# Performance work log

Measured on AMD Instinct MI355X. Metric: run time of the kernel, lower is better.

## Reference

```python
import jax, jax.numpy as jnp
import numpy as np

N_MEMBERS = 2      # ensemble_length=3, loop runs i=1..2
N_NODES = 65536    # batch_size * total_length = 32 * 2048
N_EDGES = 1_048_576
N_LAYERS = 12      # num_conv_layers
D = 64             # constant feature width (linspace 64->64)


def setup_inputs() -> dict:
    key = jax.random.key(0)
    k0, k1, k2, k3 = jax.random.split(key, 4)
    x = jax.random.normal(k0, (N_MEMBERS, N_NODES, D), dtype=jnp.float32)
    edge_index = jax.random.randint(k1, (N_MEMBERS, 2, N_EDGES), 0, N_NODES, dtype=jnp.int64)
    # GCNConv weights per member/layer; scale ~ 1/sqrt(D) for stability across 12 layers
    W = jax.random.normal(k2, (N_MEMBERS, N_LAYERS, D, D), dtype=jnp.float32) / jnp.sqrt(jnp.float32(D))
    b = jax.random.normal(k3, (N_MEMBERS, N_LAYERS, D), dtype=jnp.float32) * 0.01
    return {"x": x, "edge_index": edge_index, "W": W, "b": b}


def gcn_conv(h, src, dst, W, b):
    """PyG GCNConv: add self-loops, symmetric D^-1/2 (A+I) D^-1/2 normalization,
    linear transform, bias."""
    hw = h @ W                                                # [N, D_out]
    # degree includes the self-loop (+1)
    deg = jax.ops.segment_sum(jnp.ones((src.shape[0],), h.dtype), dst,
                              num_segments=N_NODES) + jnp.asarray(1.0, h.dtype)
    dinv = jax.lax.rsqrt(deg)                                 # [N]
    norm = dinv[src] * dinv[dst]                              # [E]
    agg = jax.ops.segment_sum(norm[:, None] * hw[src], dst, num_segments=N_NODES)
    agg = agg + (dinv * dinv)[:, None] * hw                   # self-loop term
    return agg + b


def reference(x, edge_index, W, b):
    # eval mode: F.dropout(training=False) is identity
    outs = []
    for i in range(N_MEMBERS):
        src, dst = edge_index[i, 0], edge_index[i, 1]
        h = x[i]
        for j in range(N_LAYERS - 1):
            h = jax.nn.relu(gcn_conv(h, src, dst, W[i, j], b[i, j]))
        outs.append(gcn_conv(h, src, dst, W[i, N_LAYERS - 1], b[i, N_LAYERS - 1]))
    return jnp.stack(outs)  # [N_MEMBERS, N_NODES, D]
```

## Files before the change

kernel.cpp:

```cpp
#include <hip/hip_runtime.h>
#include <hip/hip_fp16.h>
#include <math.h>

#define N_MEMBERS 2
#define N_NODES   65536
#define N_EDGES   1048576
#define N_LAYERS  12
#define D         64
#define OFF_STRIDE (N_NODES + 1)
#define NODE_MASK (N_NODES - 1)

#define NBINS       256
#define BIN_CAP     5120
#define EDGES_PER_WG 4096

typedef _Float16 f16;
typedef f16   f16x8 __attribute__((ext_vector_type(8)));
typedef float f32x4 __attribute__((ext_vector_type(4)));


__global__ __launch_bounds__(256) void bin_scatter_k(const int* __restrict__ ei,
                                                     int* __restrict__ binCursor,
                                                     unsigned int* __restrict__ binned) {
    int m = blockIdx.y;
    int t = threadIdx.x;
    int eBase = blockIdx.x * EDGES_PER_WG;
    __shared__ int hist[NBINS];
    __shared__ int base[NBINS];
    hist[t] = 0;
    __syncthreads();
    const int* srcp = ei + (size_t)(m * 2 + 0) * N_EDGES;
    const int* dstp = ei + (size_t)(m * 2 + 1) * N_EDGES;
    unsigned int pk[16];
    int bn[16], rk[16];
    #pragma unroll
    for (int i = 0; i < 16; i++) {
        int e = eBase + i * 256 + t;
        int src = srcp[e] & NODE_MASK;
        int dst = dstp[e] & NODE_MASK;
        int b = dst >> 8;
        bn[i] = b;
        pk[i] = ((unsigned)src << 8) | (unsigned)(dst & 255);
        rk[i] = atomicAdd(&hist[b], 1);
    }
    __syncthreads();
    base[t] = atomicAdd(&binCursor[m * NBINS + t], hist[t]);
    __syncthreads();
    unsigned int* bb = binned + (size_t)m * NBINS * BIN_CAP;
    #pragma unroll
    for (int i = 0; i < 16; i++) {
        int pos = base[bn[i]] + rk[i];
        if (pos < BIN_CAP)
            bb[(size_t)bn[i] * BIN_CAP + pos] = pk[i];
    }
}

__global__ __launch_bounds__(256) void scan_bins_k(const int* __restrict__ cur,
                                                   int* __restrict__ bbase) {
    int m = blockIdx.x, t = threadIdx.x;
    __shared__ int sh[256];
    int v0 = cur[m * NBINS + t];
    sh[t] = v0;
    __syncthreads();
    for (int ofs = 1; ofs < 256; ofs <<= 1) {
        int v = sh[t];
        int a = (t >= ofs) ? sh[t - ofs] : 0;
        __syncthreads();
        sh[t] = v + a;
        __syncthreads();
    }
    bbase[m * NBINS + t] = sh[t] - v0;
}

__global__ __launch_bounds__(256) void bin_build_k(const unsigned int* __restrict__ binned,
                                                   const int* __restrict__ binCursor,
                                                   const int* __restrict__ bbase,
                                                   int* __restrict__ off,
                                                   float* __restrict__ dinv,
                                                   unsigned short* __restrict__ csr_src) {
    int m = blockIdx.y, b = blockIdx.x, t = threadIdx.x;
    int cnt   = binCursor[m * NBINS + b];
    int gbase = bbase[m * NBINS + b];
    const unsigned int* bb = binned + ((size_t)m * NBINS + b) * BIN_CAP;
    __shared__ int degl[256];
    __shared__ int offl[256];
    degl[t] = 0;
    __syncthreads();
    unsigned int ed[20];
    #pragma unroll
    for (int j = 0; j < 20; j++) {
        int i = t + j * 256;
        ed[j] = 0;
        if (i < cnt) {
            unsigned int w = bb[i];
            int r = atomicAdd(&degl[w & 255], 1);
            ed[j] = w | ((unsigned)r << 24);
        }
    }
    __syncthreads();
    int myDeg = degl[t];
    offl[t] = myDeg;
    __syncthreads();
    for (int ofs = 1; ofs < 256; ofs <<= 1) {
        int v = offl[t];
        int a = (t >= ofs) ? offl[t - ofs] : 0;
        __syncthreads();
        offl[t] = v + a;
        __syncthreads();
    }
    int myOff = gbase + offl[t] - myDeg;
    int node = b * 256 + t;
    off[m * OFF_STRIDE + node] = myOff;
    if (b == NBINS - 1 && t == 255) off[m * OFF_STRIDE + N_NODES] = N_EDGES;
    dinv[m * N_NODES + node] = 1.0f / sqrtf((float)myDeg + 1.0f);
    offl[t] = myOff;
    __syncthreads();
    unsigned short* cs = csr_src + (size_t)m * N_EDGES;
    #pragma unroll
    for (int j = 0; j < 20; j++) {
        int i = t + j * 256;
        if (i < cnt) {
            int dl  = ed[j] & 255;
            int src = (ed[j] >> 8) & 0xFFFF;
            int r   = ed[j] >> 24;
            cs[offl[dl] + r] = (unsigned short)src;
        }
    }
}

__global__ __launch_bounds__(256) void prescale_k(const float* __restrict__ x,
                                                  const float* __restrict__ dinv,
                                                  __half* __restrict__ g) {
    int i = blockIdx.x * 256 + threadIdx.x;
    float dv = dinv[i >> 3];
    float4 a = ((const float4*)x)[i * 2];
    float4 b = ((const float4*)x)[i * 2 + 1];
    union { __half2 h2[4]; uint4 u; } p;
    p.h2[0] = __floats2half2_rn(dv * a.x, dv * a.y);
    p.h2[1] = __floats2half2_rn(dv * a.z, dv * a.w);
    p.h2[2] = __floats2half2_rn(dv * b.x, dv * b.y);
    p.h2[3] = __floats2half2_rn(dv * b.z, dv * b.w);
    ((uint4*)g)[i] = p.u;
}

__device__ __forceinline__ void cvt8(uint4 u, float* f) {
    const __half2* h2 = (const __half2*)&u;
    #pragma unroll
    for (int i = 0; i < 4; i++) {
        float2 t = __half22float2(h2[i]);
        f[2 * i]     = t.x;
        f[2 * i + 1] = t.y;
    }
}

__global__ __launch_bounds__(256) void aggregate_k(const __half* __restrict__ g,
                                                   __half* __restrict__ S,
                                                   const int* __restrict__ off,
                                                   const unsigned short* __restrict__ csr_src,
                                                   const float* __restrict__ dinv) {
    int bflat = blockIdx.x;
    int xcd   = bflat & 7;
    int m     = xcd >> 2;
    int slot  = ((bflat >> 3) << 2) | (xcd & 3);
    int wav   = threadIdx.x >> 6;
    int nA    = slot * 8 + wav * 2;
    int nB    = nA + 1;
    int lane = threadIdx.x & 63;
    int fg   = lane & 7;
    int sub  = lane >> 3;
    const __half*         gm = g + (size_t)m * N_NODES * D;
    const int*            ob = off + m * OFF_STRIDE;
    const unsigned short* sb = csr_src + (size_t)m * N_EDGES;

    float accA[8], accB[8];
    #pragma unroll
    for (int i = 0; i < 8; i++) { accA[i] = 0.f; accB[i] = 0.f; }

    int eA0 = ob[nA], eA1 = ob[nA + 1], eB1 = ob[nB + 1];
    int eB0 = eA1;
    #pragma unroll 2
    for (int eA = eA0, eB = eB0; (eA < eA1) || (eB < eB1); eA += 8, eB += 8) {
        int ia = eA + sub, ib = eB + sub;
        int idxA = (ia < eA1) ? ia : (eA1 - 1);
        int idxB = (ib < eB1) ? ib : (eB1 - 1);
        float wA = (ia < eA1) ? 1.0f : 0.0f;
        float wB = (ib < eB1) ? 1.0f : 0.0f;
        int sA = sb[idxA];
        int sB = sb[idxB];
        uint4 gA = *(const uint4*)(gm + (size_t)sA * D + fg * 8);
        uint4 gB = *(const uint4*)(gm + (size_t)sB * D + fg * 8);
        float fA[8], fB[8];
        cvt8(gA, fA);
        cvt8(gB, fB);
        #pragma unroll
        for (int i = 0; i < 8; i++) {
            accA[i] = fmaf(wA, fA[i], accA[i]);
            accB[i] = fmaf(wB, fB[i], accB[i]);
        }
    }
    #pragma unroll
    for (int msk = 8; msk < 64; msk <<= 1)
        #pragma unroll
        for (int i = 0; i < 8; i++) {
            accA[i] += __shfl_xor(accA[i], msk);
            accB[i] += __shfl_xor(accB[i], msk);
        }

    float dvA = dinv[m * N_NODES + nA];
    float dvB = dinv[m * N_NODES + nB];
    uint4 sgA = *(const uint4*)(gm + (size_t)nA * D + fg * 8);
    uint4 sgB = *(const uint4*)(gm + (size_t)nB * D + fg * 8);
    float sfA[8], sfB[8];
    cvt8(sgA, sfA);
    cvt8(sgB, sfB);
    __half* Sm = S + (size_t)m * N_NODES * D;
    if (sub == 0) {
        union { __half2 h2[4]; uint4 u; } p;
        #pragma unroll
        for (int i = 0; i < 4; i++)
            p.h2[i] = __floats2half2_rn(dvA * (accA[2 * i]     + sfA[2 * i]),
                                        dvA * (accA[2 * i + 1] + sfA[2 * i + 1]));
        *(uint4*)(Sm + (size_t)nA * D + fg * 8) = p.u;
    } else if (sub == 1) {
        union { __half2 h2[4]; uint4 u; } p;
        #pragma unroll
        for (int i = 0; i < 4; i++)
            p.h2[i] = __floats2half2_rn(dvB * (accB[2 * i]     + sfB[2 * i]),
                                        dvB * (accB[2 * i + 1] + sfB[2 * i + 1]));
        *(uint4*)(Sm + (size_t)nB * D + fg * 8) = p.u;
    }
}

__global__ __launch_bounds__(256) void gemm_f16_k(const __half* __restrict__ S,
                                                  const float* __restrict__ Wall,
                                                  const float* __restrict__ dinv,
                                                  const float* __restrict__ ball,
                                                  __half* __restrict__ gout,
                                                  float* __restrict__ fout,
                                                  int layer, int last) {
    int m = blockIdx.y;
    const float* Wg = Wall + (size_t)(m * N_LAYERS + layer) * D * D;
    __shared__ __align__(16) _Float16 Whi[D][72];
    __shared__ __align__(16) _Float16 Wlo[D][72];
    for (int idx = threadIdx.x; idx < D * D / 4; idx += 256) {
        float4 v = ((const float4*)Wg)[idx];
        int k  = idx >> 4;
        int c0 = (idx & 15) << 2;
        float vv[4] = {v.x, v.y, v.z, v.w};
        #pragma unroll
        for (int i = 0; i < 4; i++) {
            f16 hi = (f16)vv[i];
            Whi[c0 + i][k] = hi;
            Wlo[c0 + i][k] = (f16)(vv[i] - (float)hi);
        }
    }
    __syncthreads();

    int lane = threadIdx.x & 63;
    int wav  = threadIdx.x >> 6;
    int nn   = lane & 15;
    int quad = lane >> 4;

    f16x8 Bh[8], Bl[8];
    #pragma unroll
    for (int t = 0; t < 4; t++)
        #pragma unroll
        for (int s = 0; s < 2; s++) {
            Bh[t * 2 + s] = *(const f16x8*)&Whi[t * 16 + nn][s * 32 + quad * 8];
            Bl[t * 2 + s] = *(const f16x8*)&Wlo[t * 16 + nn][s * 32 + quad * 8];
        }

    const __half* Sm = S + (size_t)m * N_NODES * D;
    const float*  dm = dinv + m * N_NODES;
    const float*  bp = ball + (size_t)(m * N_LAYERS + layer) * D;
    __half*       gm = gout + (size_t)m * N_NODES * D;
    float*        fm = fout + (size_t)m * N_NODES * D;

    float4 b4[4];
    #pragma unroll
    for (int t = 0; t < 4; t++)
        b4[t] = *(const float4*)(bp + t * 16 + quad * 4);

    int base = blockIdx.x * 128 + wav * 32;
    #pragma unroll
    for (int g = 0; g < 2; g++) {
        int node = base + g * 16 + nn;
        const __half* srow = Sm + (size_t)node * D;
        f16x8 a0 = *(const f16x8*)(srow + quad * 8);
        f16x8 a1 = *(const f16x8*)(srow + 32 + quad * 8);
        float dv = dm[node];
        #pragma unroll
        for (int t = 0; t < 4; t++) {
            f32x4 c = {0.f, 0.f, 0.f, 0.f};
            c = __builtin_amdgcn_mfma_f32_16x16x32_f16(Bh[t * 2 + 0], a0, c, 0, 0, 0);
            c = __builtin_amdgcn_mfma_f32_16x16x32_f16(Bh[t * 2 + 1], a1, c, 0, 0, 0);
            c = __builtin_amdgcn_mfma_f32_16x16x32_f16(Bl[t * 2 + 0], a0, c, 0, 0, 0);
            c = __builtin_amdgcn_mfma_f32_16x16x32_f16(Bl[t * 2 + 1], a1, c, 0, 0, 0);
            float v0 = (float)c[0] + b4[t].x;
            float v1 = (float)c[1] + b4[t].y;
            float v2 = (float)c[2] + b4[t].z;
            float v3 = (float)c[3] + b4[t].w;
            int col = t * 16 + quad * 4;
            if (last) {
                *(float4*)(fm + (size_t)node * D + col) = make_float4(v0, v1, v2, v3);
            } else {
                union { __half2 h2[2]; uint2 u; } p;
                p.h2[0] = __floats2half2_rn(fmaxf(v0, 0.f) * dv, fmaxf(v1, 0.f) * dv);
                p.h2[1] = __floats2half2_rn(fmaxf(v2, 0.f) * dv, fmaxf(v3, 0.f) * dv);
                *(uint2*)(gm + (size_t)node * D + col) = p.u;
            }
        }
    }
}


extern "C" void kernel_launch(void* const* d_in, const int* in_sizes, int n_in,
                              void* d_out, int out_size, void* d_ws, size_t ws_size,
                              hipStream_t stream) {
    (void)in_sizes; (void)n_in; (void)out_size; (void)ws_size;
    const float* x  = (const float*)d_in[0];
    const int*   ei = (const int*)d_in[1];
    const float* W  = (const float*)d_in[2];
    const float* b  = (const float*)d_in[3];
    float* out = (float*)d_out;

    char* ws = (char*)d_ws;
    size_t o = 0;
    auto take = [&](size_t bytes) -> void* {
        void* p = ws + o;
        o = (o + bytes + 255) & ~(size_t)255;
        return p;
    };
    float*          dinv      = (float*) take((size_t)N_MEMBERS * N_NODES * 4);
    int*            off       = (int*)   take((size_t)N_MEMBERS * OFF_STRIDE * 4);
    int*            binCursor = (int*)   take((size_t)N_MEMBERS * NBINS * 4);
    int*            bbase     = (int*)   take((size_t)N_MEMBERS * NBINS * 4);
    unsigned short* csr_src   = (unsigned short*)take((size_t)N_MEMBERS * N_EDGES * 2);
    __half*         gbuf      = (__half*)take((size_t)N_MEMBERS * N_NODES * D * 2);
    __half*         Sbuf      = (__half*)take((size_t)N_MEMBERS * N_NODES * D * 2);
    unsigned int*   binned    = (unsigned int*)Sbuf;

    hipMemsetAsync(binCursor, 0, (size_t)N_MEMBERS * NBINS * 4, stream);

    bin_scatter_k<<<dim3(N_EDGES / EDGES_PER_WG, N_MEMBERS), 256, 0, stream>>>(
        ei, binCursor, binned);
    scan_bins_k<<<dim3(N_MEMBERS), 256, 0, stream>>>(binCursor, bbase);
    bin_build_k<<<dim3(NBINS, N_MEMBERS), 256, 0, stream>>>(
        binned, binCursor, bbase, off, dinv, csr_src);
    prescale_k<<<dim3((N_MEMBERS * N_NODES * D / 8) / 256), 256, 0, stream>>>(
        x, dinv, gbuf);

    for (int j = 0; j < N_LAYERS; j++) {
        aggregate_k<<<dim3(N_MEMBERS * (N_NODES / 8)), 256, 0, stream>>>(
            gbuf, Sbuf, off, csr_src, dinv);
        gemm_f16_k<<<dim3(N_NODES / 128, N_MEMBERS), 256, 0, stream>>>(
            Sbuf, W, dinv, b, gbuf, out, j, (j == N_LAYERS - 1) ? 1 : 0);
    }
}
```

Before: 806.5 us.

## Fuse aggregation and GEMM into one per-layer kernel via shared-memory tile

Merges the sparse aggregation kernel and the dense f16 MFMA GEMM into a single layer kernel. Each block aggregates 32 nodes into a shared-memory tile, then multiplies it by the split hi/lo weights and writes the activated, prescaled output to a ping-pong buffer. This removes the global write and re-read of the intermediate S buffer and halves kernel launches per layer. In exchange, every block reloads and converts the 64x64 weight matrix (2048 blocks instead of 1024), and each wave processes 8 nodes serially, which lowers latency hiding in the gather phase.

```diff
diff --git a/kernel.cpp b/kernel.cpp
--- a/kernel.cpp
+++ b/kernel.cpp
@@ -153,95 +153,26 @@
     }
 }
 
-__global__ __launch_bounds__(256) void aggregate_k(const __half* __restrict__ g,
-                                                   __half* __restrict__ S,
-                                                   const int* __restrict__ off,
-                                                   const unsigned short* __restrict__ csr_src,
-                                                   const float* __restrict__ dinv) {
+__global__ __launch_bounds__(256) void layer_k(const __half* __restrict__ g,
+                                               const float* __restrict__ Wall,
+                                               const float* __restrict__ dinv,
+                                               const float* __restrict__ ball,
+                                               const int* __restrict__ off,
+                                               const unsigned short* __restrict__ csr_src,
+                                               __half* __restrict__ gout,
+                                               float* __restrict__ fout,
+                                               int layer, int last) {
+    __shared__ __align__(16) _Float16 Whi[D][72];
+    __shared__ __align__(16) _Float16 Wlo[D][72];
+    __shared__ __align__(16) _Float16 Sl[32][72];
+
     int bflat = blockIdx.x;
     int xcd   = bflat & 7;
     int m     = xcd >> 2;
     int slot  = ((bflat >> 3) << 2) | (xcd & 3);
-    int wav   = threadIdx.x >> 6;
-    int nA    = slot * 8 + wav * 2;
-    int nB    = nA + 1;
-    int lane = threadIdx.x & 63;
-    int fg   = lane & 7;
-    int sub  = lane >> 3;
-    const __half*         gm = g + (size_t)m * N_NODES * D;
-    const int*            ob = off + m * OFF_STRIDE;
-    const unsigned short* sb = csr_src + (size_t)m * N_EDGES;
-
-    float accA[8], accB[8];
-    #pragma unroll
-    for (int i = 0; i < 8; i++) { accA[i] = 0.f; accB[i] = 0.f; }
-
-    int eA0 = ob[nA], eA1 = ob[nA + 1], eB1 = ob[nB + 1];
-    int eB0 = eA1;
-    #pragma unroll 2
-    for (int eA = eA0, eB = eB0; (eA < eA1) || (eB < eB1); eA += 8, eB += 8) {
-        int ia = eA + sub, ib = eB + sub;
-        int idxA = (ia < eA1) ? ia : (eA1 - 1);
-        int idxB = (ib < eB1) ? ib : (eB1 - 1);
-        float wA = (ia < eA1) ? 1.0f : 0.0f;
-        float wB = (ib < eB1) ? 1.0f : 0.0f;
-        int sA = sb[idxA];
-        int sB = sb[idxB];
-        uint4 gA = *(const uint4*)(gm + (size_t)sA * D + fg * 8);
-        uint4 gB = *(const uint4*)(gm + (size_t)sB * D + fg * 8);
-        float fA[8], fB[8];
-        cvt8(gA, fA);
-        cvt8(gB, fB);
-        #pragma unroll
-        for (int i = 0; i < 8; i++) {
-            accA[i] = fmaf(wA, fA[i], accA[i]);
-            accB[i] = fmaf(wB, fB[i], accB[i]);
-        }
-    }
-    #pragma unroll
-    for (int msk = 8; msk < 64; msk <<= 1)
-        #pragma unroll
-        for (int i = 0; i < 8; i++) {
-            accA[i] += __shfl_xor(accA[i], msk);
-            accB[i] += __shfl_xor(accB[i], msk);
-        }
-
-    float dvA = dinv[m * N_NODES + nA];
-    float dvB = dinv[m * N_NODES + nB];
-    uint4 sgA = *(const uint4*)(gm + (size_t)nA * D + fg * 8);
-    uint4 sgB = *(const uint4*)(gm + (size_t)nB * D + fg * 8);
-    float sfA[8], sfB[8];
-    cvt8(sgA, sfA);
-    cvt8(sgB, sfB);
-    __half* Sm = S + (size_t)m * N_NODES * D;
-    if (sub == 0) {
-        union { __half2 h2[4]; uint4 u; } p;
-        #pragma unroll
-        for (int i = 0; i < 4; i++)
-            p.h2[i] = __floats2half2_rn(dvA * (accA[2 * i]     + sfA[2 * i]),
-                                        dvA * (accA[2 * i + 1] + sfA[2 * i + 1]));
-        *(uint4*)(Sm + (size_t)nA * D + fg * 8) = p.u;
-    } else if (sub == 1) {
-        union { __half2 h2[4]; uint4 u; } p;
-        #pragma unroll
-        for (int i = 0; i < 4; i++)
-            p.h2[i] = __floats2half2_rn(dvB * (accB[2 * i]     + sfB[2 * i]),
-                                        dvB * (accB[2 * i + 1] + sfB[2 * i + 1]));
-        *(uint4*)(Sm + (size_t)nB * D + fg * 8) = p.u;
-    }
-}
-
-__global__ __launch_bounds__(256) void gemm_f16_k(const __half* __restrict__ S,
-                                                  const float* __restrict__ Wall,
-                                                  const float* __restrict__ dinv,
-                                                  const float* __restrict__ ball,
-                                                  __half* __restrict__ gout,
-                                                  float* __restrict__ fout,
-                                                  int layer, int last) {
-    int m = blockIdx.y;
+    int n0    = slot * 32;
+
     const float* Wg = Wall + (size_t)(m * N_LAYERS + layer) * D * D;
-    __shared__ __align__(16) _Float16 Whi[D][72];
-    __shared__ __align__(16) _Float16 Wlo[D][72];
     for (int idx = threadIdx.x; idx < D * D / 4; idx += 256) {
         float4 v = ((const float4*)Wg)[idx];
         int k  = idx >> 4;
@@ -254,61 +185,119 @@
             Wlo[c0 + i][k] = (f16)(vv[i] - (float)hi);
         }
     }
-    __syncthreads();
-
+
+    int wav  = threadIdx.x >> 6;
     int lane = threadIdx.x & 63;
-    int wav  = threadIdx.x >> 6;
+    int fg   = lane & 7;
+    int sub  = lane >> 3;
+    const __half*         gm = g + (size_t)m * N_NODES * D;
+    const int*            ob = off + m * OFF_STRIDE;
+    const unsigned short* sb = csr_src + (size_t)m * N_EDGES;
+
+    for (int p = 0; p < 4; p++) {
+        int nA = n0 + wav * 8 + p * 2;
+        int nB = nA + 1;
+
+        float accA[8], accB[8];
+        #pragma unroll
+        for (int i = 0; i < 8; i++) { accA[i] = 0.f; accB[i] = 0.f; }
+
+        int eA0 = ob[nA], eA1 = ob[nA + 1], eB1 = ob[nB + 1];
+        int eB0 = eA1;
+        #pragma unroll 2
+        for (int eA = eA0, eB = eB0; (eA < eA1) || (eB < eB1); eA += 8, eB += 8) {
+            int ia = eA + sub, ib = eB + sub;
+            int idxA = (ia < eA1) ? ia : (eA1 - 1);
+            int idxB = (ib < eB1) ? ib : (eB1 - 1);
+            float wA = (ia < eA1) ? 1.0f : 0.0f;
+            float wB = (ib < eB1) ? 1.0f : 0.0f;
+            int sA = sb[idxA];
+            int sB = sb[idxB];
+            uint4 gA = *(const uint4*)(gm + (size_t)sA * D + fg * 8);
+            uint4 gB = *(const uint4*)(gm + (size_t)sB * D + fg * 8);
+            float fA[8], fB[8];
+            cvt8(gA, fA);
+            cvt8(gB, fB);
+            #pragma unroll
+            for (int i = 0; i < 8; i++) {
+                accA[i] = fmaf(wA, fA[i], accA[i]);
+                accB[i] = fmaf(wB, fB[i], accB[i]);
+            }
+        }
+        #pragma unroll
+        for (int msk = 8; msk < 64; msk <<= 1)
+            #pragma unroll
+            for (int i = 0; i < 8; i++) {
+                accA[i] += __shfl_xor(accA[i], msk);
+                accB[i] += __shfl_xor(accB[i], msk);
+            }
+
+        float dvA = dinv[m * N_NODES + nA];
+        float dvB = dinv[m * N_NODES + nB];
+        uint4 sgA = *(const uint4*)(gm + (size_t)nA * D + fg * 8);
+        uint4 sgB = *(const uint4*)(gm + (size_t)nB * D + fg * 8);
+        float sfA[8], sfB[8];
+        cvt8(sgA, sfA);
+        cvt8(sgB, sfB);
+        if (sub == 0) {
+            union { __half2 h2[4]; uint4 u; } q;
+            #pragma unroll
+            for (int i = 0; i < 4; i++)
+                q.h2[i] = __floats2half2_rn(dvA * (accA[2 * i]     + sfA[2 * i]),
+                                            dvA * (accA[2 * i + 1] + sfA[2 * i + 1]));
+            *(uint4*)&Sl[nA - n0][fg * 8] = q.u;
+        } else if (sub == 1) {
+            union { __half2 h2[4]; uint4 u; } q;
+            #pragma unroll
+            for (int i = 0; i < 4; i++)
+                q.h2[i] = __floats2half2_rn(dvB * (accB[2 * i]     + sfB[2 * i]),
+                                            dvB * (accB[2 * i + 1] + sfB[2 * i + 1]));
+            *(uint4*)&Sl[nB - n0][fg * 8] = q.u;
+        }
+    }
+    __syncthreads();
+
     int nn   = lane & 15;
     int quad = lane >> 4;
-
-    f16x8 Bh[8], Bl[8];
-    #pragma unroll
-    for (int t = 0; t < 4; t++)
-        #pragma unroll
-        for (int s = 0; s < 2; s++) {
-            Bh[t * 2 + s] = *(const f16x8*)&Whi[t * 16 + nn][s * 32 + quad * 8];
-            Bl[t * 2 + s] = *(const f16x8*)&Wlo[t * 16 + nn][s * 32 + quad * 8];
-        }
-
-    const __half* Sm = S + (size_t)m * N_NODES * D;
-    const float*  dm = dinv + m * N_NODES;
-    const float*  bp = ball + (size_t)(m * N_LAYERS + layer) * D;
-    __half*       gm = gout + (size_t)m * N_NODES * D;
-    float*        fm = fout + (size_t)m * N_NODES * D;
-
-    float4 b4[4];
-    #pragma unroll
-    for (int t = 0; t < 4; t++)
-        b4[t] = *(const float4*)(bp + t * 16 + quad * 4);
-
-    int base = blockIdx.x * 128 + wav * 32;
-    #pragma unroll
-    for (int g = 0; g < 2; g++) {
-        int node = base + g * 16 + nn;
-        const __half* srow = Sm + (size_t)node * D;
-        f16x8 a0 = *(const f16x8*)(srow + quad * 8);
-        f16x8 a1 = *(const f16x8*)(srow + 32 + quad * 8);
-        float dv = dm[node];
-        #pragma unroll
-        for (int t = 0; t < 4; t++) {
-            f32x4 c = {0.f, 0.f, 0.f, 0.f};
-            c = __builtin_amdgcn_mfma_f32_16x16x32_f16(Bh[t * 2 + 0], a0, c, 0, 0, 0);
-            c = __builtin_amdgcn_mfma_f32_16x16x32_f16(Bh[t * 2 + 1], a1, c, 0, 0, 0);
-            c = __builtin_amdgcn_mfma_f32_16x16x32_f16(Bl[t * 2 + 0], a0, c, 0, 0, 0);
-            c = __builtin_amdgcn_mfma_f32_16x16x32_f16(Bl[t * 2 + 1], a1, c, 0, 0, 0);
-            float v0 = (float)c[0] + b4[t].x;
-            float v1 = (float)c[1] + b4[t].y;
-            float v2 = (float)c[2] + b4[t].z;
-            float v3 = (float)c[3] + b4[t].w;
-            int col = t * 16 + quad * 4;
-            if (last) {
-                *(float4*)(fm + (size_t)node * D + col) = make_float4(v0, v1, v2, v3);
-            } else {
-                union { __half2 h2[2]; uint2 u; } p;
-                p.h2[0] = __floats2half2_rn(fmaxf(v0, 0.f) * dv, fmaxf(v1, 0.f) * dv);
-                p.h2[1] = __floats2half2_rn(fmaxf(v2, 0.f) * dv, fmaxf(v3, 0.f) * dv);
-                *(uint2*)(gm + (size_t)node * D + col) = p.u;
-            }
+    int ng   = wav & 1;
+    int t0   = (wav >> 1) * 2;
+
+    const float* bp = ball + (size_t)(m * N_LAYERS + layer) * D;
+    __half*      gmo = gout + (size_t)m * N_NODES * D;
+    float*       fmo = fout + (size_t)m * N_NODES * D;
+
+    const _Float16* srow = &Sl[ng * 16 + nn][0];
+    f16x8 a0 = *(const f16x8*)(srow + quad * 8);
+    f16x8 a1 = *(const f16x8*)(srow + 32 + quad * 8);
+
+    int   node = n0 + ng * 16 + nn;
+    float dv   = dinv[m * N_NODES + node];
+
+    #pragma unroll
+    for (int tt = 0; tt < 2; tt++) {
+        int t = t0 + tt;
+        f16x8 Bh0 = *(const f16x8*)&Whi[t * 16 + nn][quad * 8];
+        f16x8 Bh1 = *(const f16x8*)&Whi[t * 16 + nn][32 + quad * 8];
+        f16x8 Bl0 = *(const f16x8*)&Wlo[t * 16 + nn][quad * 8];
+        f16x8 Bl1 = *(const f16x8*)&Wlo[t * 16 + nn][32 + quad * 8];
+        f32x4 c = {0.f, 0.f, 0.f, 0.f};
+        c = __builtin_amdgcn_mfma_f32_16x16x32_f16(Bh0, a0, c, 0, 0, 0);
+        c = __builtin_amdgcn_mfma_f32_16x16x32_f16(Bh1, a1, c, 0, 0, 0);
+        c = __builtin_amdgcn_mfma_f32_16x16x32_f16(Bl0, a0, c, 0, 0, 0);
+        c = __builtin_amdgcn_mfma_f32_16x16x32_f16(Bl1, a1, c, 0, 0, 0);
+        float4 b4 = *(const float4*)(bp + t * 16 + quad * 4);
+        float v0 = (float)c[0] + b4.x;
+        float v1 = (float)c[1] + b4.y;
+        float v2 = (float)c[2] + b4.z;
+        float v3 = (float)c[3] + b4.w;
+        int col = t * 16 + quad * 4;
+        if (last) {
+            *(float4*)(fmo + (size_t)node * D + col) = make_float4(v0, v1, v2, v3);
+        } else {
+            union { __half2 h2[2]; uint2 u; } p;
+            p.h2[0] = __floats2half2_rn(fmaxf(v0, 0.f) * dv, fmaxf(v1, 0.f) * dv);
+            p.h2[1] = __floats2half2_rn(fmaxf(v2, 0.f) * dv, fmaxf(v3, 0.f) * dv);
+            *(uint2*)(gmo + (size_t)node * D + col) = p.u;
         }
     }
 }
@@ -336,9 +325,9 @@
     int*            binCursor = (int*)   take((size_t)N_MEMBERS * NBINS * 4);
     int*            bbase     = (int*)   take((size_t)N_MEMBERS * NBINS * 4);
     unsigned short* csr_src   = (unsigned short*)take((size_t)N_MEMBERS * N_EDGES * 2);
-    __half*         gbuf      = (__half*)take((size_t)N_MEMBERS * N_NODES * D * 2);
-    __half*         Sbuf      = (__half*)take((size_t)N_MEMBERS * N_NODES * D * 2);
-    unsigned int*   binned    = (unsigned int*)Sbuf;
+    __half*         g0        = (__half*)take((size_t)N_MEMBERS * N_NODES * D * 2);
+    __half*         g1        = (__half*)take((size_t)N_MEMBERS * N_NODES * D * 2);
+    unsigned int*   binned    = (unsigned int*)g1;
 
     hipMemsetAsync(binCursor, 0, (size_t)N_MEMBERS * NBINS * 4, stream);
 
@@ -348,12 +337,13 @@
     bin_build_k<<<dim3(NBINS, N_MEMBERS), 256, 0, stream>>>(
         binned, binCursor, bbase, off, dinv, csr_src);
     prescale_k<<<dim3((N_MEMBERS * N_NODES * D / 8) / 256), 256, 0, stream>>>(
-        x, dinv, gbuf);
-
+        x, dinv, g0);
+
+    __half* gin  = g0;
+    __half* gout_ = g1;
     for (int j = 0; j < N_LAYERS; j++) {
-        aggregate_k<<<dim3(N_MEMBERS * (N_NODES / 8)), 256, 0, stream>>>(
-            gbuf, Sbuf, off, csr_src, dinv);
-        gemm_f16_k<<<dim3(N_NODES / 128, N_MEMBERS), 256, 0, stream>>>(
-            Sbuf, W, dinv, b, gbuf, out, j, (j == N_LAYERS - 1) ? 1 : 0);
-    }
-}
+        layer_k<<<dim3(N_MEMBERS * (N_NODES / 32)), 256, 0, stream>>>(
+            gin, W, dinv, b, off, csr_src, gout_, out, j, (j == N_LAYERS - 1) ? 1 : 0);
+        __half* tmp = gin; gin = gout_; gout_ = tmp;
+    }
+}
```

Measured after the change: 892.2 us. 1.11x slower.

## Presplit weights into MFMA fragment layout once and add nontemporal loads/stores

Applied to the files above, without the earlier changes.

A new kernel converts every layer's fp32 weights into hi/lo fp16 fragments once, stored in the exact per-lane MFMA register order. The GEMM kernel then loads these fragments straight from global memory instead of rebuilding them in shared memory with a barrier in every block. The GEMM also handles 256 nodes per block instead of 128, so each block spreads the fragment load over more work. Nontemporal hints are added to the CSR index loads and to the S and output stores to reduce cache pollution.

```diff
diff --git a/kernel.cpp b/kernel.cpp
--- a/kernel.cpp
+++ b/kernel.cpp
@@ -17,6 +17,7 @@
 typedef _Float16 f16;
 typedef f16   f16x8 __attribute__((ext_vector_type(8)));
 typedef float f32x4 __attribute__((ext_vector_type(4)));
+typedef unsigned int u32x4 __attribute__((ext_vector_type(4)));
 
 
 __global__ __launch_bounds__(256) void bin_scatter_k(const int* __restrict__ ei,
@@ -128,6 +129,32 @@
     }
 }
 
+__global__ __launch_bounds__(256) void presplit_k(const float* __restrict__ Wall,
+                                                  __half* __restrict__ Wsplit) {
+    int gid = blockIdx.x * 256 + threadIdx.x;
+    int ml   = gid >> 9;
+    int r    = gid & 511;
+    int t    = (r >> 7) & 3;
+    int s    = (r >> 6) & 1;
+    int lane = r & 63;
+    int c  = t * 16 + (lane & 15);
+    int k0 = s * 32 + (lane >> 4) * 8;
+    const float* Wg = Wall + (size_t)ml * D * D;
+    __half* base = Wsplit + (size_t)ml * 8192;
+    int fo = ((t * 2 + s) * 64 + lane) * 8;
+    __half hi8[8], lo8[8];
+    #pragma unroll
+    for (int j = 0; j < 8; j++) {
+        float v = Wg[(k0 + j) * D + c];
+        f16 h = (f16)v;
+        hi8[j] = *(__half*)&h;
+        f16 l = (f16)(v - (float)h);
+        lo8[j] = *(__half*)&l;
+    }
+    *(uint4*)(base + fo)        = *(uint4*)hi8;
+    *(uint4*)(base + 4096 + fo) = *(uint4*)lo8;
+}
+
 __global__ __launch_bounds__(256) void prescale_k(const float* __restrict__ x,
                                                   const float* __restrict__ dinv,
                                                   __half* __restrict__ g) {
@@ -151,6 +178,17 @@
         f[2 * i]     = t.x;
         f[2 * i + 1] = t.y;
     }
+}
+
+__device__ __forceinline__ u32x4 pack_s(const float* acc, const float* sf, float dv) {
+    u32x4 v;
+    #pragma unroll
+    for (int i = 0; i < 4; i++) {
+        __half2 h = __floats2half2_rn(dv * (acc[2 * i]     + sf[2 * i]),
+                                      dv * (acc[2 * i + 1] + sf[2 * i + 1]));
+        v[i] = *(unsigned int*)&h;
+    }
+    return v;
 }
 
 __global__ __launch_bounds__(256) void aggregate_k(const __half* __restrict__ g,
@@ -185,8 +223,8 @@
         int idxB = (ib < eB1) ? ib : (eB1 - 1);
         float wA = (ia < eA1) ? 1.0f : 0.0f;
         float wB = (ib < eB1) ? 1.0f : 0.0f;
-        int sA = sb[idxA];
-        int sB = sb[idxB];
+        int sA = __builtin_nontemporal_load(&sb[idxA]);
+        int sB = __builtin_nontemporal_load(&sb[idxB]);
         uint4 gA = *(const uint4*)(gm + (size_t)sA * D + fg * 8);
         uint4 gB = *(const uint4*)(gm + (size_t)sB * D + fg * 8);
         float fA[8], fB[8];
@@ -215,59 +253,36 @@
     cvt8(sgB, sfB);
     __half* Sm = S + (size_t)m * N_NODES * D;
     if (sub == 0) {
-        union { __half2 h2[4]; uint4 u; } p;
-        #pragma unroll
-        for (int i = 0; i < 4; i++)
-            p.h2[i] = __floats2half2_rn(dvA * (accA[2 * i]     + sfA[2 * i]),
-                                        dvA * (accA[2 * i + 1] + sfA[2 * i + 1]));
-        *(uint4*)(Sm + (size_t)nA * D + fg * 8) = p.u;
+        u32x4 v = pack_s(accA, sfA, dvA);
+        __builtin_nontemporal_store(v, (u32x4*)(Sm + (size_t)nA * D + fg * 8));
     } else if (sub == 1) {
-        union { __half2 h2[4]; uint4 u; } p;
-        #pragma unroll
-        for (int i = 0; i < 4; i++)
-            p.h2[i] = __floats2half2_rn(dvB * (accB[2 * i]     + sfB[2 * i]),
-                                        dvB * (accB[2 * i + 1] + sfB[2 * i + 1]));
-        *(uint4*)(Sm + (size_t)nB * D + fg * 8) = p.u;
+        u32x4 v = pack_s(accB, sfB, dvB);
+        __builtin_nontemporal_store(v, (u32x4*)(Sm + (size_t)nB * D + fg * 8));
     }
 }
 
 __global__ __launch_bounds__(256) void gemm_f16_k(const __half* __restrict__ S,
-                                                  const float* __restrict__ Wall,
+                                                  const __half* __restrict__ Wsplit,
                                                   const float* __restrict__ dinv,
                                                   const float* __restrict__ ball,
                                                   __half* __restrict__ gout,
                                                   float* __restrict__ fout,
                                                   int layer, int last) {
     int m = blockIdx.y;
-    const float* Wg = Wall + (size_t)(m * N_LAYERS + layer) * D * D;
-    __shared__ __align__(16) _Float16 Whi[D][72];
-    __shared__ __align__(16) _Float16 Wlo[D][72];
-    for (int idx = threadIdx.x; idx < D * D / 4; idx += 256) {
-        float4 v = ((const float4*)Wg)[idx];
-        int k  = idx >> 4;
-        int c0 = (idx & 15) << 2;
-        float vv[4] = {v.x, v.y, v.z, v.w};
-        #pragma unroll
-        for (int i = 0; i < 4; i++) {
-            f16 hi = (f16)vv[i];
-            Whi[c0 + i][k] = hi;
-            Wlo[c0 + i][k] = (f16)(vv[i] - (float)hi);
-        }
-    }
-    __syncthreads();
-
     int lane = threadIdx.x & 63;
     int wav  = threadIdx.x >> 6;
     int nn   = lane & 15;
     int quad = lane >> 4;
 
+    const __half* Wf = Wsplit + (size_t)(m * N_LAYERS + layer) * 8192;
     f16x8 Bh[8], Bl[8];
     #pragma unroll
     for (int t = 0; t < 4; t++)
         #pragma unroll
         for (int s = 0; s < 2; s++) {
-            Bh[t * 2 + s] = *(const f16x8*)&Whi[t * 16 + nn][s * 32 + quad * 8];
-            Bl[t * 2 + s] = *(const f16x8*)&Wlo[t * 16 + nn][s * 32 + quad * 8];
+            int fo = ((t * 2 + s) * 64 + lane) * 8;
+            Bh[t * 2 + s] = *(const f16x8*)(Wf + fo);
+            Bl[t * 2 + s] = *(const f16x8*)(Wf + 4096 + fo);
         }
 
     const __half* Sm = S + (size_t)m * N_NODES * D;
@@ -281,9 +296,9 @@
     for (int t = 0; t < 4; t++)
         b4[t] = *(const float4*)(bp + t * 16 + quad * 4);
 
-    int base = blockIdx.x * 128 + wav * 32;
-    #pragma unroll
-    for (int g = 0; g < 2; g++) {
+    int base = blockIdx.x * 256 + wav * 64;
+    #pragma unroll
+    for (int g = 0; g < 4; g++) {
         int node = base + g * 16 + nn;
         const __half* srow = Sm + (size_t)node * D;
         f16x8 a0 = *(const f16x8*)(srow + quad * 8);
@@ -302,7 +317,8 @@
             float v3 = (float)c[3] + b4[t].w;
             int col = t * 16 + quad * 4;
             if (last) {
-                *(float4*)(fm + (size_t)node * D + col) = make_float4(v0, v1, v2, v3);
+                f32x4 v = {v0, v1, v2, v3};
+                __builtin_nontemporal_store(v, (f32x4*)(fm + (size_t)node * D + col));
             } else {
                 union { __half2 h2[2]; uint2 u; } p;
                 p.h2[0] = __floats2half2_rn(fmaxf(v0, 0.f) * dv, fmaxf(v1, 0.f) * dv);
@@ -336,12 +352,14 @@
     int*            binCursor = (int*)   take((size_t)N_MEMBERS * NBINS * 4);
     int*            bbase     = (int*)   take((size_t)N_MEMBERS * NBINS * 4);
     unsigned short* csr_src   = (unsigned short*)take((size_t)N_MEMBERS * N_EDGES * 2);
+    __half*         Wsplit    = (__half*)take((size_t)N_MEMBERS * N_LAYERS * 8192 * 2);
     __half*         gbuf      = (__half*)take((size_t)N_MEMBERS * N_NODES * D * 2);
     __half*         Sbuf      = (__half*)take((size_t)N_MEMBERS * N_NODES * D * 2);
     unsigned int*   binned    = (unsigned int*)Sbuf;
 
     hipMemsetAsync(binCursor, 0, (size_t)N_MEMBERS * NBINS * 4, stream);
 
+    presplit_k<<<dim3(N_MEMBERS * N_LAYERS * 512 / 256), 256, 0, stream>>>(W, Wsplit);
     bin_scatter_k<<<dim3(N_EDGES / EDGES_PER_WG, N_MEMBERS), 256, 0, stream>>>(
         ei, binCursor, binned);
     scan_bins_k<<<dim3(N_MEMBERS), 256, 0, stream>>>(binCursor, bbase);
@@ -353,7 +371,7 @@
     for (int j = 0; j < N_LAYERS; j++) {
         aggregate_k<<<dim3(N_MEMBERS * (N_NODES / 8)), 256, 0, stream>>>(
             gbuf, Sbuf, off, csr_src, dinv);
-        gemm_f16_k<<<dim3(N_NODES / 128, N_MEMBERS), 256, 0, stream>>>(
-            Sbuf, W, dinv, b, gbuf, out, j, (j == N_LAYERS - 1) ? 1 : 0);
-    }
-}
+        gemm_f16_k<<<dim3(N_NODES / 256, N_MEMBERS), 256, 0, stream>>>(
+            Sbuf, Wsplit, dinv, b, gbuf, out, j, (j == N_LAYERS - 1) ? 1 : 0);
+    }
+}
```

Measured after the change: 877.0 us. 8.7% more time.
